# Kernel tuning notes

Measured on AMD Instinct MI355X. Metric: run time of the kernel, lower is better.

## Reference

```python
import jax, jax.numpy as jnp
import numpy as np

D_MODEL = 256
NHEAD = 8
HEAD_DIM = D_MODEL // NHEAD
EPS_ATTN = 1e-6
EPS_LN = 1e-5


def layer_norm(x, g, b):
    mu = jnp.mean(x, axis=-1, keepdims=True)
    var = jnp.mean(jnp.square(x - mu), axis=-1, keepdims=True)
    return (x - mu) * jax.lax.rsqrt(var + EPS_LN) * g + b


def setup_inputs() -> dict:
    key = jax.random.key(0)
    ks = jax.random.split(key, 9)
    N, L, S = 8, 8192, 8192
    d = D_MODEL
    sc = 1.0 / np.sqrt(d)
    return {
        "x": jax.random.normal(ks[0], (N, L, d), dtype=jnp.float32),
        "source": jax.random.normal(ks[1], (N, S, d), dtype=jnp.float32),
        "Wq": jax.random.normal(ks[2], (d, d), dtype=jnp.float32) * sc,
        "Wk": jax.random.normal(ks[3], (d, d), dtype=jnp.float32) * sc,
        "Wv": jax.random.normal(ks[4], (d, d), dtype=jnp.float32) * sc,
        "Wm": jax.random.normal(ks[5], (d, d), dtype=jnp.float32) * sc,
        "W1": jax.random.normal(ks[6], (2 * d, d), dtype=jnp.float32) * (1.0 / np.sqrt(2 * d)),
        "W2": jax.random.normal(ks[7], (d, d), dtype=jnp.float32) * sc,
        "g1": jnp.ones((d,), jnp.float32),
        "b1": jnp.zeros((d,), jnp.float32),
        "g2": jnp.ones((d,), jnp.float32),
        "b2": jnp.zeros((d,), jnp.float32),
    }


def linear_attention(q, k, v):
    # q: [N,L,H,D], k,v: [N,S,H,D]
    Q = jax.nn.elu(q) + 1.0
    K = jax.nn.elu(k) + 1.0
    S = v.shape[1]
    v = v / S
    KV = jnp.einsum('nshd,nshv->nhdv', K, v)          # [N,H,D,D]
    Z = 1.0 / (jnp.einsum('nlhd,nhd->nlh', Q, K.sum(axis=1)) + EPS_ATTN)
    out = jnp.einsum('nlhd,nhdv,nlh->nlhv', Q, KV, Z) * S
    return out


def reference(x, source, Wq, Wk, Wv, Wm, W1, W2, g1, b1, g2, b2):
    N, L, _ = x.shape
    q = (x @ Wq).reshape(N, L, NHEAD, HEAD_DIM)
    k = (source @ Wk).reshape(N, -1, NHEAD, HEAD_DIM)
    v = (source @ Wv).reshape(N, -1, NHEAD, HEAD_DIM)
    msg = linear_attention(q, k, v).reshape(N, L, D_MODEL)
    msg = layer_norm(msg @ Wm, g1, b1)
    msg = jnp.concatenate([x, msg], axis=2)
    msg = jax.nn.relu(msg @ W1) @ W2
    msg = layer_norm(msg, g2, b2)
    return x + msg
```

## Files before the change

kernel.cpp:

```cpp
#include <hip/hip_runtime.h>

typedef __attribute__((ext_vector_type(4))) float f32x4;
typedef __attribute__((ext_vector_type(8))) short short8;
typedef __attribute__((ext_vector_type(4))) unsigned short us4;
typedef __attribute__((ext_vector_type(8))) unsigned short us8;

#define D_MODEL 256
#define SEQ 8192L
#define NBATCH 8
#define TOTROWS 65536L

__device__ inline unsigned short f2bf(float f){
  unsigned int u = __float_as_uint(f);
  u += 0x7fffu + ((u >> 16) & 1u);
  return (unsigned short)(u >> 16);
}
__device__ inline float bf2f(unsigned short h){
  return __uint_as_float(((unsigned int)h) << 16);
}
__device__ inline f32x4 mfma16(short8 a, short8 b, f32x4 c){
  return __builtin_amdgcn_mfma_f32_16x16x32_bf16(a, b, c, 0, 0, 0);
}
__device__ inline us8 pack8(f32x4 a, f32x4 b){
  us8 o;
  o[0]=f2bf(a[0]); o[1]=f2bf(a[1]); o[2]=f2bf(a[2]); o[3]=f2bf(a[3]);
  o[4]=f2bf(b[0]); o[5]=f2bf(b[1]); o[6]=f2bf(b[2]); o[7]=f2bf(b[3]);
  return o;
}
__device__ inline void gl16(const unsigned short* g, unsigned short* lds){
  __builtin_amdgcn_global_load_lds(
      (const __attribute__((address_space(1))) unsigned int*)g,
      (__attribute__((address_space(3))) unsigned int*)lds, 16, 0, 0);
}

__global__ __launch_bounds__(256) void conv_f32_to_bf16(
    const float* __restrict__ s, unsigned short* __restrict__ d){
  const long N = TOTROWS * 256 / 8;
  for(long c = (long)blockIdx.x * 256 + threadIdx.x; c < N;
      c += (long)gridDim.x * 256){
    long off = c * 8;
    f32x4 v0 = *(const f32x4*)(s + off);
    f32x4 v1 = *(const f32x4*)(s + off + 4);
    *(us8*)(d + off) = pack8(v0, v1);
  }
}

__global__ void prep_weights(const float* __restrict__ Wq, const float* __restrict__ Wk,
                             const float* __restrict__ Wv, const float* __restrict__ Wm,
                             const float* __restrict__ W1, const float* __restrict__ W2,
                             unsigned short* __restrict__ WT){
  int o = blockIdx.x * 256 + threadIdx.x;
  int m = o >> 16, rem = o & 65535, n = rem >> 8, k = rem & 255;
  const float* s;
  switch(m){
    case 0: s = Wq; break;
    case 1: s = Wk; break;
    case 2: s = Wv; break;
    case 3: s = Wm; break;
    case 4: s = W1; break;
    case 5: s = W1 + 65536; break;
    default: s = W2; break;
  }
  WT[o] = f2bf(s[k * 256 + n]);
}

__global__ __launch_bounds__(256) void kv_proj(
    const unsigned short* __restrict__ srcb, const unsigned short* __restrict__ WT,
    unsigned short* __restrict__ Kw, unsigned short* __restrict__ Vw)
{
  __shared__ unsigned short As[128][32];
  __shared__ unsigned short Bs[128][32];
  const int t = threadIdx.x, lane = t & 63, wid = t >> 6;
  const int l16 = lane & 15, g4 = lane >> 4;
  const int wr = (wid >> 1) * 64, wc = (wid & 1) * 64;
  const int mb = blockIdx.x, nb = blockIdx.y;
  const long rowbase = (long)mb * 128;
  const unsigned short* Wsl = WT + (nb < 2 ? 1 : 2) * 65536 + (nb & 1) * 128 * 256;
  const int sr = lane >> 2, sc = (lane & 3) * 8;

  f32x4 acc[4][4] = {};
  for(int kb = 0; kb < 256; kb += 32){
    #pragma unroll
    for(int j = 0; j < 2; j++){
      int r0 = wid * 32 + j * 16;
      gl16(srcb + (rowbase + r0 + sr) * 256 + kb + sc, &As[r0][0]);
      gl16(Wsl  + (long)(r0 + sr) * 256 + kb + sc,     &Bs[r0][0]);
    }
    __syncthreads();
    short8 afr[4], bfr[4];
    #pragma unroll
    for(int mi = 0; mi < 4; mi++) afr[mi] = *(const short8*)&As[wr + mi*16 + l16][g4*8];
    #pragma unroll
    for(int ni = 0; ni < 4; ni++) bfr[ni] = *(const short8*)&Bs[wc + ni*16 + l16][g4*8];
    #pragma unroll
    for(int mi = 0; mi < 4; mi++)
      #pragma unroll
      for(int ni = 0; ni < 4; ni++)
        acc[mi][ni] = mfma16(afr[mi], bfr[ni], acc[mi][ni]);
    __syncthreads();
  }

  const bool isK = nb < 2;
  unsigned short* dst = isK ? Kw : Vw;
  const int colbase = (nb & 1) * 128 + wc;
  #pragma unroll
  for(int mi = 0; mi < 4; mi++)
    #pragma unroll
    for(int ni = 0; ni < 4; ni++)
      #pragma unroll
      for(int rr = 0; rr < 4; rr++){
        long row = rowbase + wr + mi*16 + g4*4 + rr;
        int col = colbase + ni*16 + l16;
        float v = acc[mi][ni][rr];
        v = isK ? (v > 0.f ? v + 1.f : __expf(v)) : v * (1.f / 8192.f);
        dst[row * 256 + col] = f2bf(v);
      }
}

__global__ __launch_bounds__(256) void kv_acc(const unsigned short* __restrict__ Kw,
                                              const unsigned short* __restrict__ Vw,
                                              float* __restrict__ part){
  const int c = blockIdx.x;
  const int n = blockIdx.y;
  const int t = threadIdx.x;
  const int h = t >> 5, d = t & 31;
  const long base = ((long)n * SEQ + (long)c * 128) * 256;
  float acc[32];
  #pragma unroll
  for(int j = 0; j < 32; j++) acc[j] = 0.f;
  float ks = 0.f;
  for(int rr = 0; rr < 128; rr++){
    const unsigned short* Kr = Kw + base + (long)rr * 256;
    const unsigned short* Vr = Vw + base + (long)rr * 256;
    float kv = bf2f(Kr[h * 32 + d]);
    ks += kv;
    #pragma unroll
    for(int q = 0; q < 4; q++){
      us8 vv = *(const us8*)(Vr + h * 32 + q * 8);
      #pragma unroll
      for(int j = 0; j < 8; j++) acc[q*8 + j] += kv * bf2f(vv[j]);
    }
  }
  float* p = part + ((long)(n * 64 + c) * 33) * 256;
  #pragma unroll
  for(int v = 0; v < 32; v++) p[v * 256 + t] = acc[v];
  p[32 * 256 + t] = ks;
}

__global__ void kv_red(const float* __restrict__ part, float* __restrict__ KVws){
  const int v = blockIdx.x;
  const int n = blockIdx.y;
  const int t = threadIdx.x;
  float s = 0.f;
  for(int c = 0; c < 64; c++) s += part[((long)(n * 64 + c) * 33 + v) * 256 + t];
  KVws[((long)n * 33 + v) * 256 + t] = s;
}

__global__ __launch_bounds__(256) void attn_kern(
    const unsigned short* __restrict__ xb, const unsigned short* __restrict__ WT,
    const float* __restrict__ KVws, const float* __restrict__ g1,
    const float* __restrict__ b1, unsigned short* __restrict__ msgln)
{
  __shared__ unsigned short As[64][32];
  __shared__ unsigned short Bu[256][32];
  __shared__ float zs[64][8];
  __shared__ float ksl[256];
  __shared__ unsigned short R[64][264];

  const int t = threadIdx.x, lane = t & 63, wid = t >> 6;
  const int l16 = lane & 15, g4 = lane >> 4;
  const int wc = wid * 64;
  const int mb = blockIdx.x;
  const long rowbase = (long)mb * 64;
  const int n = mb >> 7;
  const int sr = lane >> 2, sc = (lane & 3) * 8;

  f32x4 acc[4][4] = {};
  {
    const unsigned short* wq = WT;
    for(int kb = 0; kb < 256; kb += 32){
      gl16(xb + (rowbase + wid*16 + sr) * 256 + kb + sc, &As[wid*16][0]);
      #pragma unroll
      for(int j = 0; j < 4; j++){
        int r0 = wid * 64 + j * 16;
        gl16(wq + (long)(r0 + sr) * 256 + kb + sc, &Bu[r0][0]);
      }
      __syncthreads();
      short8 afr[4], bfr[4];
      #pragma unroll
      for(int mi = 0; mi < 4; mi++) afr[mi] = *(const short8*)&As[mi*16 + l16][g4*8];
      #pragma unroll
      for(int ni = 0; ni < 4; ni++) bfr[ni] = *(const short8*)&Bu[wc + ni*16 + l16][g4*8];
      #pragma unroll
      for(int mi = 0; mi < 4; mi++)
        #pragma unroll
        for(int ni = 0; ni < 4; ni++)
          acc[mi][ni] = mfma16(afr[mi], bfr[ni], acc[mi][ni]);
      __syncthreads();
    }
  }

  #pragma unroll
  for(int mi = 0; mi < 4; mi++)
    #pragma unroll
    for(int ni = 0; ni < 4; ni++)
      #pragma unroll
      for(int rr = 0; rr < 4; rr++){
        float v = acc[mi][ni][rr];
        v = v > 0.f ? v + 1.f : __expf(v);
        R[mi*16 + g4*4 + rr][wc + ni*16 + l16] = f2bf(v);
      }

  {
    const float* kvn = KVws + (long)n * 33 * 256;
    const int vv = t & 31, hh = t >> 5;
    #pragma unroll
    for(int d = 0; d < 32; d += 4){
      f32x4 w = *(const f32x4*)(kvn + vv * 256 + hh * 32 + d);
      us4 o; o[0]=f2bf(w[0]); o[1]=f2bf(w[1]); o[2]=f2bf(w[2]); o[3]=f2bf(w[3]);
      *(us4*)&Bu[t][d] = o;
    }
    ksl[t] = kvn[32 * 256 + t];
  }
  __syncthreads();

  #pragma unroll
  for(int pp = 0; pp < 2; pp++){
    int p = t + pp * 256;
    int row = p >> 3, h = p & 7;
    float s = 0.f;
    #pragma unroll
    for(int d = 0; d < 32; d++) s += bf2f(R[row][h*32 + d]) * ksl[h*32 + d];
    zs[row][h] = 1.f / (s + 1e-6f);
  }
  __syncthreads();

  f32x4 acc2[4][4];
  #pragma unroll
  for(int ni = 0; ni < 4; ni++){
    const int cb = wc + ni * 16;
    const int h = cb >> 5;
    short8 b = *(const short8*)&Bu[cb + l16][g4*8];
    #pragma unroll
    for(int mi = 0; mi < 4; mi++){
      short8 a = *(const short8*)&R[mi*16 + l16][h*32 + g4*8];
      f32x4 zz = {0.f, 0.f, 0.f, 0.f};
      acc2[mi][ni] = mfma16(a, b, zz);
    }
  }
  #pragma unroll
  for(int mi = 0; mi < 4; mi++)
    #pragma unroll
    for(int ni = 0; ni < 4; ni++){
      const int h = (wc + ni * 16) >> 5;
      #pragma unroll
      for(int rr = 0; rr < 4; rr++){
        int row = mi*16 + g4*4 + rr;
        acc2[mi][ni][rr] *= zs[row][h] * 8192.f;
      }
    }
  __syncthreads();
  #pragma unroll
  for(int mi = 0; mi < 4; mi++)
    #pragma unroll
    for(int ni = 0; ni < 4; ni++)
      #pragma unroll
      for(int rr = 0; rr < 4; rr++)
        R[mi*16 + g4*4 + rr][wc + ni*16 + l16] = f2bf(acc2[mi][ni][rr]);
  __syncthreads();

  f32x4 acc3[4][4] = {};
  {
    const unsigned short* wm = WT + 3 * 65536;
    for(int kb = 0; kb < 256; kb += 32){
      #pragma unroll
      for(int j = 0; j < 4; j++){
        int r0 = wid * 64 + j * 16;
        gl16(wm + (long)(r0 + sr) * 256 + kb + sc, &Bu[r0][0]);
      }
      __syncthreads();
      short8 afr[4], bfr[4];
      #pragma unroll
      for(int mi = 0; mi < 4; mi++) afr[mi] = *(const short8*)&R[mi*16 + l16][kb + g4*8];
      #pragma unroll
      for(int ni = 0; ni < 4; ni++) bfr[ni] = *(const short8*)&Bu[wc + ni*16 + l16][g4*8];
      #pragma unroll
      for(int mi = 0; mi < 4; mi++)
        #pragma unroll
        for(int ni = 0; ni < 4; ni++)
          acc3[mi][ni] = mfma16(afr[mi], bfr[ni], acc3[mi][ni]);
      __syncthreads();
    }
  }

  #pragma unroll
  for(int mi = 0; mi < 4; mi++)
    #pragma unroll
    for(int ni = 0; ni < 4; ni++)
      #pragma unroll
      for(int rr = 0; rr < 4; rr++)
        R[mi*16 + g4*4 + rr][wc + ni*16 + l16] = f2bf(acc3[mi][ni][rr]);
  __syncthreads();

  {
    int row = t >> 2, q = t & 3;
    float s = 0.f, ss = 0.f;
    #pragma unroll
    for(int j8 = 0; j8 < 8; j8++){
      us8 vv = *(const us8*)&R[row][q*64 + j8*8];
      #pragma unroll
      for(int e = 0; e < 8; e++){ float v = bf2f(vv[e]); s += v; ss += v * v; }
    }
    s  += __shfl_xor(s, 1);  ss += __shfl_xor(ss, 1);
    s  += __shfl_xor(s, 2);  ss += __shfl_xor(ss, 2);
    float mu  = s * (1.f / 256.f);
    float var = ss * (1.f / 256.f) - mu * mu;
    float rs  = rsqrtf(var + 1e-5f);
    unsigned short* orow = msgln + (rowbase + row) * 256 + q * 64;
    const float* g1p = g1 + q * 64;
    const float* b1p = b1 + q * 64;
    #pragma unroll
    for(int j8 = 0; j8 < 8; j8++){
      us8 vv = *(const us8*)&R[row][q*64 + j8*8];
      us8 o;
      #pragma unroll
      for(int e = 0; e < 8; e++){
        float v = (bf2f(vv[e]) - mu) * rs * g1p[j8*8 + e] + b1p[j8*8 + e];
        o[e] = f2bf(v);
      }
      *(us8*)(orow + j8*8) = o;
    }
  }
}

__global__ __launch_bounds__(256) void ffn_kern(
    const float* __restrict__ x, const unsigned short* __restrict__ xb,
    const unsigned short* __restrict__ WT,
    const unsigned short* __restrict__ msgln, const float* __restrict__ g2,
    const float* __restrict__ b2, float* __restrict__ out)
{
  __shared__ unsigned short As[64][32];
  __shared__ unsigned short Bs[256][32];
  __shared__ unsigned short R[64][264];
  const int t = threadIdx.x, lane = t & 63, wid = t >> 6;
  const int l16 = lane & 15, g4 = lane >> 4;
  const int wc = wid * 64;
  const long rowbase = (long)blockIdx.x * 64;
  const int sr = lane >> 2, sc = (lane & 3) * 8;

  f32x4 acc[4][4] = {};
  for(int it = 0; it < 16; it++){
    int kb = (it & 7) * 32;
    const unsigned short* asrc = (it < 8) ? xb : msgln;
    gl16(asrc + (rowbase + wid*16 + sr) * 256 + kb + sc, &As[wid*16][0]);
    const unsigned short* wsl = WT + (it < 8 ? 4 : 5) * 65536;
    #pragma unroll
    for(int j = 0; j < 4; j++){
      int r0 = wid * 64 + j * 16;
      gl16(wsl + (long)(r0 + sr) * 256 + kb + sc, &Bs[r0][0]);
    }
    __syncthreads();
    short8 afr[4], bfr[4];
    #pragma unroll
    for(int mi = 0; mi < 4; mi++) afr[mi] = *(const short8*)&As[mi*16 + l16][g4*8];
    #pragma unroll
    for(int ni = 0; ni < 4; ni++) bfr[ni] = *(const short8*)&Bs[wc + ni*16 + l16][g4*8];
    #pragma unroll
    for(int mi = 0; mi < 4; mi++)
      #pragma unroll
      for(int ni = 0; ni < 4; ni++)
        acc[mi][ni] = mfma16(afr[mi], bfr[ni], acc[mi][ni]);
    __syncthreads();
  }

  #pragma unroll
  for(int mi = 0; mi < 4; mi++)
    #pragma unroll
    for(int ni = 0; ni < 4; ni++)
      #pragma unroll
      for(int rr = 0; rr < 4; rr++){
        float v = acc[mi][ni][rr];
        R[mi*16 + g4*4 + rr][wc + ni*16 + l16] = f2bf(v > 0.f ? v : 0.f);
      }
  __syncthreads();

  f32x4 acc2[4][4] = {};
  {
    const unsigned short* w2 = WT + 6 * 65536;
    for(int kb = 0; kb < 256; kb += 32){
      #pragma unroll
      for(int j = 0; j < 4; j++){
        int r0 = wid * 64 + j * 16;
        gl16(w2 + (long)(r0 + sr) * 256 + kb + sc, &Bs[r0][0]);
      }
      __syncthreads();
      short8 afr[4], bfr[4];
      #pragma unroll
      for(int mi = 0; mi < 4; mi++) afr[mi] = *(const short8*)&R[mi*16 + l16][kb + g4*8];
      #pragma unroll
      for(int ni = 0; ni < 4; ni++) bfr[ni] = *(const short8*)&Bs[wc + ni*16 + l16][g4*8];
      #pragma unroll
      for(int mi = 0; mi < 4; mi++)
        #pragma unroll
        for(int ni = 0; ni < 4; ni++)
          acc2[mi][ni] = mfma16(afr[mi], bfr[ni], acc2[mi][ni]);
      __syncthreads();
    }
  }

  #pragma unroll
  for(int mi = 0; mi < 4; mi++)
    #pragma unroll
    for(int ni = 0; ni < 4; ni++)
      #pragma unroll
      for(int rr = 0; rr < 4; rr++)
        R[mi*16 + g4*4 + rr][wc + ni*16 + l16] = f2bf(acc2[mi][ni][rr]);
  __syncthreads();

  {
    int row = t >> 2, q = t & 3;
    float s = 0.f, ss = 0.f;
    #pragma unroll
    for(int j8 = 0; j8 < 8; j8++){
      us8 vv = *(const us8*)&R[row][q*64 + j8*8];
      #pragma unroll
      for(int e = 0; e < 8; e++){ float v = bf2f(vv[e]); s += v; ss += v * v; }
    }
    s  += __shfl_xor(s, 1);  ss += __shfl_xor(ss, 1);
    s  += __shfl_xor(s, 2);  ss += __shfl_xor(ss, 2);
    float mu  = s * (1.f / 256.f);
    float var = ss * (1.f / 256.f) - mu * mu;
    float rs  = rsqrtf(var + 1e-5f);
    const float* xr = x + (rowbase + row) * 256 + q * 64;
    float* orow = out + (rowbase + row) * 256 + q * 64;
    const float* g2p = g2 + q * 64;
    const float* b2p = b2 + q * 64;
    #pragma unroll
    for(int j4 = 0; j4 < 16; j4++){
      f32x4 xv = *(const f32x4*)(xr + j4 * 4);
      f32x4 o;
      #pragma unroll
      for(int e = 0; e < 4; e++){
        int idx = j4 * 4 + e;
        float v = (bf2f(R[row][q*64 + idx]) - mu) * rs * g2p[idx] + b2p[idx];
        o[e] = xv[e] + v;
      }
      *(f32x4*)(orow + j4 * 4) = o;
    }
  }
}

extern "C" void kernel_launch(void* const* d_in, const int* in_sizes, int n_in,
                              void* d_out, int out_size, void* d_ws, size_t ws_size,
                              hipStream_t stream)
{
  const float* x   = (const float*)d_in[0];
  const float* src = (const float*)d_in[1];
  const float* Wq  = (const float*)d_in[2];
  const float* Wk  = (const float*)d_in[3];
  const float* Wv  = (const float*)d_in[4];
  const float* Wm  = (const float*)d_in[5];
  const float* W1  = (const float*)d_in[6];
  const float* W2  = (const float*)d_in[7];
  const float* g1  = (const float*)d_in[8];
  const float* b1  = (const float*)d_in[9];
  const float* g2  = (const float*)d_in[10];
  const float* b2  = (const float*)d_in[11];

  char* ws = (char*)d_ws;
  unsigned short* WT   = (unsigned short*)(ws);
  unsigned short* srcb = (unsigned short*)(ws + (1ul  << 20));
  float*          part = (float*)         (ws + (1ul  << 20));
  unsigned short* xb   = (unsigned short*)(ws + (1ul  << 20));
  unsigned short* Kw   = (unsigned short*)(ws + (33ul << 20));
  unsigned short* msgl = Kw;
  unsigned short* Vw   = (unsigned short*)(ws + (65ul << 20));
  float*          KVws = (float*)         (ws + (97ul << 20));

  prep_weights<<<1792, 256, 0, stream>>>(Wq, Wk, Wv, Wm, W1, W2, WT);
  conv_f32_to_bf16<<<2048, 256, 0, stream>>>(src, srcb);
  kv_proj<<<dim3(512, 4), 256, 0, stream>>>(srcb, WT, Kw, Vw);
  kv_acc<<<dim3(64, 8), 256, 0, stream>>>(Kw, Vw, part);
  kv_red<<<dim3(33, 8), 256, 0, stream>>>(part, KVws);
  conv_f32_to_bf16<<<2048, 256, 0, stream>>>(x, xb);
  attn_kern<<<1024, 256, 0, stream>>>(xb, WT, KVws, g1, b1, msgl);
  ffn_kern<<<1024, 256, 0, stream>>>(x, xb, WT, msgl, g2, b2, (float*)d_out);
}
```

Baseline: 415.8 us.

## Double-buffer LDS tiles in projection, attention and FFN GEMM loops

Converts the k-loops of kv_proj, attn_kern and ffn_kern to a two-buffer shared-memory pipeline. Each iteration issues the next tile's global-to-LDS loads into the other buffer before doing the MFMAs on the current one, which removes one barrier per iteration. The Wm and W2 tiles for the second GEMM are prefetched during the preceding epilogue. This roughly doubles the staging LDS per block, which may lower occupancy, especially in attn_kern.

```diff
diff --git a/kernel.cpp b/kernel.cpp
--- a/kernel.cpp
+++ b/kernel.cpp
@@ -68,8 +68,8 @@
     const unsigned short* __restrict__ srcb, const unsigned short* __restrict__ WT,
     unsigned short* __restrict__ Kw, unsigned short* __restrict__ Vw)
 {
-  __shared__ unsigned short As[128][32];
-  __shared__ unsigned short Bs[128][32];
+  __shared__ unsigned short As[2][128][32];
+  __shared__ unsigned short Bs[2][128][32];
   const int t = threadIdx.x, lane = t & 63, wid = t >> 6;
   const int l16 = lane & 15, g4 = lane >> 4;
   const int wr = (wid >> 1) * 64, wc = (wid & 1) * 64;
@@ -78,26 +78,33 @@
   const unsigned short* Wsl = WT + (nb < 2 ? 1 : 2) * 65536 + (nb & 1) * 128 * 256;
   const int sr = lane >> 2, sc = (lane & 3) * 8;
 
-  f32x4 acc[4][4] = {};
-  for(int kb = 0; kb < 256; kb += 32){
+  auto STAGE = [&](int buf, int kb){
     #pragma unroll
     for(int j = 0; j < 2; j++){
       int r0 = wid * 32 + j * 16;
-      gl16(srcb + (rowbase + r0 + sr) * 256 + kb + sc, &As[r0][0]);
-      gl16(Wsl  + (long)(r0 + sr) * 256 + kb + sc,     &Bs[r0][0]);
-    }
-    __syncthreads();
+      gl16(srcb + (rowbase + r0 + sr) * 256 + kb + sc, &As[buf][r0][0]);
+      gl16(Wsl  + (long)(r0 + sr) * 256 + kb + sc,     &Bs[buf][r0][0]);
+    }
+  };
+
+  f32x4 acc[4][4] = {};
+  STAGE(0, 0);
+  __syncthreads();
+  int cur = 0;
+  for(int it = 0; it < 8; it++){
+    if(it < 7) STAGE(cur ^ 1, (it + 1) * 32);
     short8 afr[4], bfr[4];
     #pragma unroll
-    for(int mi = 0; mi < 4; mi++) afr[mi] = *(const short8*)&As[wr + mi*16 + l16][g4*8];
-    #pragma unroll
-    for(int ni = 0; ni < 4; ni++) bfr[ni] = *(const short8*)&Bs[wc + ni*16 + l16][g4*8];
+    for(int mi = 0; mi < 4; mi++) afr[mi] = *(const short8*)&As[cur][wr + mi*16 + l16][g4*8];
+    #pragma unroll
+    for(int ni = 0; ni < 4; ni++) bfr[ni] = *(const short8*)&Bs[cur][wc + ni*16 + l16][g4*8];
     #pragma unroll
     for(int mi = 0; mi < 4; mi++)
       #pragma unroll
       for(int ni = 0; ni < 4; ni++)
         acc[mi][ni] = mfma16(afr[mi], bfr[ni], acc[mi][ni]);
     __syncthreads();
+    cur ^= 1;
   }
 
   const bool isK = nb < 2;
@@ -161,8 +168,8 @@
     const float* __restrict__ KVws, const float* __restrict__ g1,
     const float* __restrict__ b1, unsigned short* __restrict__ msgln)
 {
-  __shared__ unsigned short As[64][32];
-  __shared__ unsigned short Bu[256][32];
+  __shared__ unsigned short As[2][64][32];
+  __shared__ unsigned short Bu[2][256][32];
   __shared__ float zs[64][8];
   __shared__ float ksl[256];
   __shared__ unsigned short R[64][264];
@@ -175,29 +182,43 @@
   const int n = mb >> 7;
   const int sr = lane >> 2, sc = (lane & 3) * 8;
 
+  const unsigned short* wq = WT;
+  const unsigned short* wm = WT + 3 * 65536;
+
+  auto STAGE1 = [&](int buf, int kb){
+    gl16(xb + (rowbase + wid*16 + sr) * 256 + kb + sc, &As[buf][wid*16][0]);
+    #pragma unroll
+    for(int j = 0; j < 4; j++){
+      int r0 = wid * 64 + j * 16;
+      gl16(wq + (long)(r0 + sr) * 256 + kb + sc, &Bu[buf][r0][0]);
+    }
+  };
+  auto STAGE6 = [&](int buf, int kb){
+    #pragma unroll
+    for(int j = 0; j < 4; j++){
+      int r0 = wid * 64 + j * 16;
+      gl16(wm + (long)(r0 + sr) * 256 + kb + sc, &Bu[buf][r0][0]);
+    }
+  };
+
   f32x4 acc[4][4] = {};
-  {
-    const unsigned short* wq = WT;
-    for(int kb = 0; kb < 256; kb += 32){
-      gl16(xb + (rowbase + wid*16 + sr) * 256 + kb + sc, &As[wid*16][0]);
-      #pragma unroll
-      for(int j = 0; j < 4; j++){
-        int r0 = wid * 64 + j * 16;
-        gl16(wq + (long)(r0 + sr) * 256 + kb + sc, &Bu[r0][0]);
-      }
-      __syncthreads();
-      short8 afr[4], bfr[4];
-      #pragma unroll
-      for(int mi = 0; mi < 4; mi++) afr[mi] = *(const short8*)&As[mi*16 + l16][g4*8];
-      #pragma unroll
-      for(int ni = 0; ni < 4; ni++) bfr[ni] = *(const short8*)&Bu[wc + ni*16 + l16][g4*8];
-      #pragma unroll
-      for(int mi = 0; mi < 4; mi++)
-        #pragma unroll
-        for(int ni = 0; ni < 4; ni++)
-          acc[mi][ni] = mfma16(afr[mi], bfr[ni], acc[mi][ni]);
-      __syncthreads();
-    }
+  STAGE1(0, 0);
+  __syncthreads();
+  int cur = 0;
+  for(int it = 0; it < 8; it++){
+    if(it < 7) STAGE1(cur ^ 1, (it + 1) * 32);
+    short8 afr[4], bfr[4];
+    #pragma unroll
+    for(int mi = 0; mi < 4; mi++) afr[mi] = *(const short8*)&As[cur][mi*16 + l16][g4*8];
+    #pragma unroll
+    for(int ni = 0; ni < 4; ni++) bfr[ni] = *(const short8*)&Bu[cur][wc + ni*16 + l16][g4*8];
+    #pragma unroll
+    for(int mi = 0; mi < 4; mi++)
+      #pragma unroll
+      for(int ni = 0; ni < 4; ni++)
+        acc[mi][ni] = mfma16(afr[mi], bfr[ni], acc[mi][ni]);
+    __syncthreads();
+    cur ^= 1;
   }
 
   #pragma unroll
@@ -218,7 +239,7 @@
     for(int d = 0; d < 32; d += 4){
       f32x4 w = *(const f32x4*)(kvn + vv * 256 + hh * 32 + d);
       us4 o; o[0]=f2bf(w[0]); o[1]=f2bf(w[1]); o[2]=f2bf(w[2]); o[3]=f2bf(w[3]);
-      *(us4*)&Bu[t][d] = o;
+      *(us4*)&Bu[0][t][d] = o;
     }
     ksl[t] = kvn[32 * 256 + t];
   }
@@ -240,7 +261,7 @@
   for(int ni = 0; ni < 4; ni++){
     const int cb = wc + ni * 16;
     const int h = cb >> 5;
-    short8 b = *(const short8*)&Bu[cb + l16][g4*8];
+    short8 b = *(const short8*)&Bu[0][cb + l16][g4*8];
     #pragma unroll
     for(int mi = 0; mi < 4; mi++){
       short8 a = *(const short8*)&R[mi*16 + l16][h*32 + g4*8];
@@ -248,6 +269,7 @@
       acc2[mi][ni] = mfma16(a, b, zz);
     }
   }
+  STAGE6(1, 0);
   #pragma unroll
   for(int mi = 0; mi < 4; mi++)
     #pragma unroll
@@ -270,27 +292,22 @@
   __syncthreads();
 
   f32x4 acc3[4][4] = {};
-  {
-    const unsigned short* wm = WT + 3 * 65536;
-    for(int kb = 0; kb < 256; kb += 32){
-      #pragma unroll
-      for(int j = 0; j < 4; j++){
-        int r0 = wid * 64 + j * 16;
-        gl16(wm + (long)(r0 + sr) * 256 + kb + sc, &Bu[r0][0]);
-      }
-      __syncthreads();
-      short8 afr[4], bfr[4];
-      #pragma unroll
-      for(int mi = 0; mi < 4; mi++) afr[mi] = *(const short8*)&R[mi*16 + l16][kb + g4*8];
-      #pragma unroll
-      for(int ni = 0; ni < 4; ni++) bfr[ni] = *(const short8*)&Bu[wc + ni*16 + l16][g4*8];
-      #pragma unroll
-      for(int mi = 0; mi < 4; mi++)
-        #pragma unroll
-        for(int ni = 0; ni < 4; ni++)
-          acc3[mi][ni] = mfma16(afr[mi], bfr[ni], acc3[mi][ni]);
-      __syncthreads();
-    }
+  cur = 1;
+  for(int it = 0; it < 8; it++){
+    if(it < 7) STAGE6(cur ^ 1, (it + 1) * 32);
+    int kb = it * 32;
+    short8 afr[4], bfr[4];
+    #pragma unroll
+    for(int mi = 0; mi < 4; mi++) afr[mi] = *(const short8*)&R[mi*16 + l16][kb + g4*8];
+    #pragma unroll
+    for(int ni = 0; ni < 4; ni++) bfr[ni] = *(const short8*)&Bu[cur][wc + ni*16 + l16][g4*8];
+    #pragma unroll
+    for(int mi = 0; mi < 4; mi++)
+      #pragma unroll
+      for(int ni = 0; ni < 4; ni++)
+        acc3[mi][ni] = mfma16(afr[mi], bfr[ni], acc3[mi][ni]);
+    __syncthreads();
+    cur ^= 1;
   }
 
   #pragma unroll
@@ -339,8 +356,8 @@
     const unsigned short* __restrict__ msgln, const float* __restrict__ g2,
     const float* __restrict__ b2, float* __restrict__ out)
 {
-  __shared__ unsigned short As[64][32];
-  __shared__ unsigned short Bs[256][32];
+  __shared__ unsigned short As[2][64][32];
+  __shared__ unsigned short Bs[2][256][32];
   __shared__ unsigned short R[64][264];
   const int t = threadIdx.x, lane = t & 63, wid = t >> 6;
   const int l16 = lane & 15, g4 = lane >> 4;
@@ -348,30 +365,46 @@
   const long rowbase = (long)blockIdx.x * 64;
   const int sr = lane >> 2, sc = (lane & 3) * 8;
 
-  f32x4 acc[4][4] = {};
-  for(int it = 0; it < 16; it++){
+  auto STAGE1 = [&](int buf, int it){
     int kb = (it & 7) * 32;
     const unsigned short* asrc = (it < 8) ? xb : msgln;
-    gl16(asrc + (rowbase + wid*16 + sr) * 256 + kb + sc, &As[wid*16][0]);
+    gl16(asrc + (rowbase + wid*16 + sr) * 256 + kb + sc, &As[buf][wid*16][0]);
     const unsigned short* wsl = WT + (it < 8 ? 4 : 5) * 65536;
     #pragma unroll
     for(int j = 0; j < 4; j++){
       int r0 = wid * 64 + j * 16;
-      gl16(wsl + (long)(r0 + sr) * 256 + kb + sc, &Bs[r0][0]);
-    }
-    __syncthreads();
+      gl16(wsl + (long)(r0 + sr) * 256 + kb + sc, &Bs[buf][r0][0]);
+    }
+  };
+  const unsigned short* w2 = WT + 6 * 65536;
+  auto STAGE2 = [&](int buf, int kb){
+    #pragma unroll
+    for(int j = 0; j < 4; j++){
+      int r0 = wid * 64 + j * 16;
+      gl16(w2 + (long)(r0 + sr) * 256 + kb + sc, &Bs[buf][r0][0]);
+    }
+  };
+
+  f32x4 acc[4][4] = {};
+  STAGE1(0, 0);
+  __syncthreads();
+  int cur = 0;
+  for(int it = 0; it < 16; it++){
+    if(it < 15) STAGE1(cur ^ 1, it + 1);
     short8 afr[4], bfr[4];
     #pragma unroll
-    for(int mi = 0; mi < 4; mi++) afr[mi] = *(const short8*)&As[mi*16 + l16][g4*8];
-    #pragma unroll
-    for(int ni = 0; ni < 4; ni++) bfr[ni] = *(const short8*)&Bs[wc + ni*16 + l16][g4*8];
+    for(int mi = 0; mi < 4; mi++) afr[mi] = *(const short8*)&As[cur][mi*16 + l16][g4*8];
+    #pragma unroll
+    for(int ni = 0; ni < 4; ni++) bfr[ni] = *(const short8*)&Bs[cur][wc + ni*16 + l16][g4*8];
     #pragma unroll
     for(int mi = 0; mi < 4; mi++)
       #pragma unroll
       for(int ni = 0; ni < 4; ni++)
         acc[mi][ni] = mfma16(afr[mi], bfr[ni], acc[mi][ni]);
     __syncthreads();
-  }
+    cur ^= 1;
+  }
+  STAGE2(0, 0);
 
   #pragma unroll
   for(int mi = 0; mi < 4; mi++)
@@ -385,27 +418,22 @@
   __syncthreads();
 
   f32x4 acc2[4][4] = {};
-  {
-    const unsigned short* w2 = WT + 6 * 65536;
-    for(int kb = 0; kb < 256; kb += 32){
-      #pragma unroll
-      for(int j = 0; j < 4; j++){
-        int r0 = wid * 64 + j * 16;
-        gl16(w2 + (long)(r0 + sr) * 256 + kb + sc, &Bs[r0][0]);
-      }
-      __syncthreads();
-      short8 afr[4], bfr[4];
-      #pragma unroll
-      for(int mi = 0; mi < 4; mi++) afr[mi] = *(const short8*)&R[mi*16 + l16][kb + g4*8];
-      #pragma unroll
-      for(int ni = 0; ni < 4; ni++) bfr[ni] = *(const short8*)&Bs[wc + ni*16 + l16][g4*8];
-      #pragma unroll
-      for(int mi = 0; mi < 4; mi++)
-        #pragma unroll
-        for(int ni = 0; ni < 4; ni++)
-          acc2[mi][ni] = mfma16(afr[mi], bfr[ni], acc2[mi][ni]);
-      __syncthreads();
-    }
+  cur = 0;
+  for(int it = 0; it < 8; it++){
+    if(it < 7) STAGE2(cur ^ 1, (it + 1) * 32);
+    int kb = it * 32;
+    short8 afr[4], bfr[4];
+    #pragma unroll
+    for(int mi = 0; mi < 4; mi++) afr[mi] = *(const short8*)&R[mi*16 + l16][kb + g4*8];
+    #pragma unroll
+    for(int ni = 0; ni < 4; ni++) bfr[ni] = *(const short8*)&Bs[cur][wc + ni*16 + l16][g4*8];
+    #pragma unroll
+    for(int mi = 0; mi < 4; mi++)
+      #pragma unroll
+      for(int ni = 0; ni < 4; ni++)
+        acc2[mi][ni] = mfma16(afr[mi], bfr[ni], acc2[mi][ni]);
+    __syncthreads();
+    cur ^= 1;
   }
 
   #pragma unroll
```

Result: no change. 419.9 us (+1.0%).

## Load GEMM operand fragments directly from global memory instead of LDS staging

Applied to the files above, without the earlier changes.

Replaces the global_load_lds staging of A and B tiles into shared memory in kv_proj, attn_kern and ffn_kern. Each wave now loads its MFMA fragments straight from global memory into registers inside fully unrolled K loops, with no per-iteration barriers. This drops LDS traffic and synchronisation and lets the compiler schedule loads across iterations. In exchange, each wave re-reads the weight and activation data it used to share through LDS (more cache and global traffic), makes strided 16-byte row accesses, and raises register pressure from the unrolling.

```diff
diff --git a/kernel.cpp b/kernel.cpp
--- a/kernel.cpp
+++ b/kernel.cpp
@@ -27,10 +27,8 @@
   o[4]=f2bf(b[0]); o[5]=f2bf(b[1]); o[6]=f2bf(b[2]); o[7]=f2bf(b[3]);
   return o;
 }
-__device__ inline void gl16(const unsigned short* g, unsigned short* lds){
-  __builtin_amdgcn_global_load_lds(
-      (const __attribute__((address_space(1))) unsigned int*)g,
-      (__attribute__((address_space(3))) unsigned int*)lds, 16, 0, 0);
+__device__ inline short8 g16(const unsigned short* p){
+  return *(const short8*)p;
 }
 
 __global__ __launch_bounds__(256) void conv_f32_to_bf16(
@@ -68,36 +66,29 @@
     const unsigned short* __restrict__ srcb, const unsigned short* __restrict__ WT,
     unsigned short* __restrict__ Kw, unsigned short* __restrict__ Vw)
 {
-  __shared__ unsigned short As[128][32];
-  __shared__ unsigned short Bs[128][32];
   const int t = threadIdx.x, lane = t & 63, wid = t >> 6;
   const int l16 = lane & 15, g4 = lane >> 4;
   const int wr = (wid >> 1) * 64, wc = (wid & 1) * 64;
   const int mb = blockIdx.x, nb = blockIdx.y;
   const long rowbase = (long)mb * 128;
   const unsigned short* Wsl = WT + (nb < 2 ? 1 : 2) * 65536 + (nb & 1) * 128 * 256;
-  const int sr = lane >> 2, sc = (lane & 3) * 8;
 
   f32x4 acc[4][4] = {};
-  for(int kb = 0; kb < 256; kb += 32){
-    #pragma unroll
-    for(int j = 0; j < 2; j++){
-      int r0 = wid * 32 + j * 16;
-      gl16(srcb + (rowbase + r0 + sr) * 256 + kb + sc, &As[r0][0]);
-      gl16(Wsl  + (long)(r0 + sr) * 256 + kb + sc,     &Bs[r0][0]);
-    }
-    __syncthreads();
-    short8 afr[4], bfr[4];
-    #pragma unroll
-    for(int mi = 0; mi < 4; mi++) afr[mi] = *(const short8*)&As[wr + mi*16 + l16][g4*8];
-    #pragma unroll
-    for(int ni = 0; ni < 4; ni++) bfr[ni] = *(const short8*)&Bs[wc + ni*16 + l16][g4*8];
+  #pragma unroll
+  for(int it = 0; it < 8; it++){
+    int kb = it * 32;
+    short8 a[4], b[4];
+    #pragma unroll
+    for(int mi = 0; mi < 4; mi++)
+      a[mi] = g16(srcb + (rowbase + wr + mi*16 + l16) * 256 + kb + g4*8);
+    #pragma unroll
+    for(int ni = 0; ni < 4; ni++)
+      b[ni] = g16(Wsl + (long)(wc + ni*16 + l16) * 256 + kb + g4*8);
     #pragma unroll
     for(int mi = 0; mi < 4; mi++)
       #pragma unroll
       for(int ni = 0; ni < 4; ni++)
-        acc[mi][ni] = mfma16(afr[mi], bfr[ni], acc[mi][ni]);
-    __syncthreads();
+        acc[mi][ni] = mfma16(a[mi], b[ni], acc[mi][ni]);
   }
 
   const bool isK = nb < 2;
@@ -161,8 +152,7 @@
     const float* __restrict__ KVws, const float* __restrict__ g1,
     const float* __restrict__ b1, unsigned short* __restrict__ msgln)
 {
-  __shared__ unsigned short As[64][32];
-  __shared__ unsigned short Bu[256][32];
+  __shared__ unsigned short kvB[256][32];
   __shared__ float zs[64][8];
   __shared__ float ksl[256];
   __shared__ unsigned short R[64][264];
@@ -173,31 +163,38 @@
   const int mb = blockIdx.x;
   const long rowbase = (long)mb * 64;
   const int n = mb >> 7;
-  const int sr = lane >> 2, sc = (lane & 3) * 8;
+
+  const unsigned short* wq = WT;
+  const unsigned short* wm = WT + 3 * 65536;
+
+  {
+    const float* kvn = KVws + (long)n * 33 * 256;
+    const int vv = t & 31, hh = t >> 5;
+    #pragma unroll
+    for(int d = 0; d < 32; d += 4){
+      f32x4 w = *(const f32x4*)(kvn + vv * 256 + hh * 32 + d);
+      us4 o; o[0]=f2bf(w[0]); o[1]=f2bf(w[1]); o[2]=f2bf(w[2]); o[3]=f2bf(w[3]);
+      *(us4*)&kvB[t][d] = o;
+    }
+    ksl[t] = kvn[32 * 256 + t];
+  }
 
   f32x4 acc[4][4] = {};
-  {
-    const unsigned short* wq = WT;
-    for(int kb = 0; kb < 256; kb += 32){
-      gl16(xb + (rowbase + wid*16 + sr) * 256 + kb + sc, &As[wid*16][0]);
-      #pragma unroll
-      for(int j = 0; j < 4; j++){
-        int r0 = wid * 64 + j * 16;
-        gl16(wq + (long)(r0 + sr) * 256 + kb + sc, &Bu[r0][0]);
-      }
-      __syncthreads();
-      short8 afr[4], bfr[4];
-      #pragma unroll
-      for(int mi = 0; mi < 4; mi++) afr[mi] = *(const short8*)&As[mi*16 + l16][g4*8];
-      #pragma unroll
-      for(int ni = 0; ni < 4; ni++) bfr[ni] = *(const short8*)&Bu[wc + ni*16 + l16][g4*8];
-      #pragma unroll
-      for(int mi = 0; mi < 4; mi++)
-        #pragma unroll
-        for(int ni = 0; ni < 4; ni++)
-          acc[mi][ni] = mfma16(afr[mi], bfr[ni], acc[mi][ni]);
-      __syncthreads();
-    }
+  #pragma unroll
+  for(int it = 0; it < 8; it++){
+    int kb = it * 32;
+    short8 a[4], b[4];
+    #pragma unroll
+    for(int mi = 0; mi < 4; mi++)
+      a[mi] = g16(xb + (rowbase + mi*16 + l16) * 256 + kb + g4*8);
+    #pragma unroll
+    for(int ni = 0; ni < 4; ni++)
+      b[ni] = g16(wq + (long)(wc + ni*16 + l16) * 256 + kb + g4*8);
+    #pragma unroll
+    for(int mi = 0; mi < 4; mi++)
+      #pragma unroll
+      for(int ni = 0; ni < 4; ni++)
+        acc[mi][ni] = mfma16(a[mi], b[ni], acc[mi][ni]);
   }
 
   #pragma unroll
@@ -210,18 +207,6 @@
         v = v > 0.f ? v + 1.f : __expf(v);
         R[mi*16 + g4*4 + rr][wc + ni*16 + l16] = f2bf(v);
       }
-
-  {
-    const float* kvn = KVws + (long)n * 33 * 256;
-    const int vv = t & 31, hh = t >> 5;
-    #pragma unroll
-    for(int d = 0; d < 32; d += 4){
-      f32x4 w = *(const f32x4*)(kvn + vv * 256 + hh * 32 + d);
-      us4 o; o[0]=f2bf(w[0]); o[1]=f2bf(w[1]); o[2]=f2bf(w[2]); o[3]=f2bf(w[3]);
-      *(us4*)&Bu[t][d] = o;
-    }
-    ksl[t] = kvn[32 * 256 + t];
-  }
   __syncthreads();
 
   #pragma unroll
@@ -240,7 +225,7 @@
   for(int ni = 0; ni < 4; ni++){
     const int cb = wc + ni * 16;
     const int h = cb >> 5;
-    short8 b = *(const short8*)&Bu[cb + l16][g4*8];
+    short8 b = *(const short8*)&kvB[cb + l16][g4*8];
     #pragma unroll
     for(int mi = 0; mi < 4; mi++){
       short8 a = *(const short8*)&R[mi*16 + l16][h*32 + g4*8];
@@ -270,28 +255,23 @@
   __syncthreads();
 
   f32x4 acc3[4][4] = {};
-  {
-    const unsigned short* wm = WT + 3 * 65536;
-    for(int kb = 0; kb < 256; kb += 32){
-      #pragma unroll
-      for(int j = 0; j < 4; j++){
-        int r0 = wid * 64 + j * 16;
-        gl16(wm + (long)(r0 + sr) * 256 + kb + sc, &Bu[r0][0]);
-      }
-      __syncthreads();
-      short8 afr[4], bfr[4];
-      #pragma unroll
-      for(int mi = 0; mi < 4; mi++) afr[mi] = *(const short8*)&R[mi*16 + l16][kb + g4*8];
-      #pragma unroll
-      for(int ni = 0; ni < 4; ni++) bfr[ni] = *(const short8*)&Bu[wc + ni*16 + l16][g4*8];
-      #pragma unroll
-      for(int mi = 0; mi < 4; mi++)
-        #pragma unroll
-        for(int ni = 0; ni < 4; ni++)
-          acc3[mi][ni] = mfma16(afr[mi], bfr[ni], acc3[mi][ni]);
-      __syncthreads();
-    }
-  }
+  #pragma unroll
+  for(int it = 0; it < 8; it++){
+    int kb = it * 32;
+    short8 afr[4], b[4];
+    #pragma unroll
+    for(int mi = 0; mi < 4; mi++)
+      afr[mi] = *(const short8*)&R[mi*16 + l16][kb + g4*8];
+    #pragma unroll
+    for(int ni = 0; ni < 4; ni++)
+      b[ni] = g16(wm + (long)(wc + ni*16 + l16) * 256 + kb + g4*8);
+    #pragma unroll
+    for(int mi = 0; mi < 4; mi++)
+      #pragma unroll
+      for(int ni = 0; ni < 4; ni++)
+        acc3[mi][ni] = mfma16(afr[mi], b[ni], acc3[mi][ni]);
+  }
+  __syncthreads();
 
   #pragma unroll
   for(int mi = 0; mi < 4; mi++)
@@ -339,38 +319,32 @@
     const unsigned short* __restrict__ msgln, const float* __restrict__ g2,
     const float* __restrict__ b2, float* __restrict__ out)
 {
-  __shared__ unsigned short As[64][32];
-  __shared__ unsigned short Bs[256][32];
   __shared__ unsigned short R[64][264];
   const int t = threadIdx.x, lane = t & 63, wid = t >> 6;
   const int l16 = lane & 15, g4 = lane >> 4;
   const int wc = wid * 64;
   const long rowbase = (long)blockIdx.x * 64;
-  const int sr = lane >> 2, sc = (lane & 3) * 8;
+
+  const unsigned short* w2 = WT + 6 * 65536;
 
   f32x4 acc[4][4] = {};
+  #pragma unroll
   for(int it = 0; it < 16; it++){
     int kb = (it & 7) * 32;
     const unsigned short* asrc = (it < 8) ? xb : msgln;
-    gl16(asrc + (rowbase + wid*16 + sr) * 256 + kb + sc, &As[wid*16][0]);
     const unsigned short* wsl = WT + (it < 8 ? 4 : 5) * 65536;
-    #pragma unroll
-    for(int j = 0; j < 4; j++){
-      int r0 = wid * 64 + j * 16;
-      gl16(wsl + (long)(r0 + sr) * 256 + kb + sc, &Bs[r0][0]);
-    }
-    __syncthreads();
-    short8 afr[4], bfr[4];
-    #pragma unroll
-    for(int mi = 0; mi < 4; mi++) afr[mi] = *(const short8*)&As[mi*16 + l16][g4*8];
-    #pragma unroll
-    for(int ni = 0; ni < 4; ni++) bfr[ni] = *(const short8*)&Bs[wc + ni*16 + l16][g4*8];
+    short8 a[4], b[4];
+    #pragma unroll
+    for(int mi = 0; mi < 4; mi++)
+      a[mi] = g16(asrc + (rowbase + mi*16 + l16) * 256 + kb + g4*8);
+    #pragma unroll
+    for(int ni = 0; ni < 4; ni++)
+      b[ni] = g16(wsl + (long)(wc + ni*16 + l16) * 256 + kb + g4*8);
     #pragma unroll
     for(int mi = 0; mi < 4; mi++)
       #pragma unroll
       for(int ni = 0; ni < 4; ni++)
-        acc[mi][ni] = mfma16(afr[mi], bfr[ni], acc[mi][ni]);
-    __syncthreads();
+        acc[mi][ni] = mfma16(a[mi], b[ni], acc[mi][ni]);
   }
 
   #pragma unroll
@@ -385,28 +359,23 @@
   __syncthreads();
 
   f32x4 acc2[4][4] = {};
-  {
-    const unsigned short* w2 = WT + 6 * 65536;
-    for(int kb = 0; kb < 256; kb += 32){
-      #pragma unroll
-      for(int j = 0; j < 4; j++){
-        int r0 = wid * 64 + j * 16;
-        gl16(w2 + (long)(r0 + sr) * 256 + kb + sc, &Bs[r0][0]);
-      }
-      __syncthreads();
-      short8 afr[4], bfr[4];
-      #pragma unroll
-      for(int mi = 0; mi < 4; mi++) afr[mi] = *(const short8*)&R[mi*16 + l16][kb + g4*8];
-      #pragma unroll
-      for(int ni = 0; ni < 4; ni++) bfr[ni] = *(const short8*)&Bs[wc + ni*16 + l16][g4*8];
-      #pragma unroll
-      for(int mi = 0; mi < 4; mi++)
-        #pragma unroll
-        for(int ni = 0; ni < 4; ni++)
-          acc2[mi][ni] = mfma16(afr[mi], bfr[ni], acc2[mi][ni]);
-      __syncthreads();
-    }
-  }
+  #pragma unroll
+  for(int it = 0; it < 8; it++){
+    int kb = it * 32;
+    short8 afr[4], b[4];
+    #pragma unroll
+    for(int mi = 0; mi < 4; mi++)
+      afr[mi] = *(const short8*)&R[mi*16 + l16][kb + g4*8];
+    #pragma unroll
+    for(int ni = 0; ni < 4; ni++)
+      b[ni] = g16(w2 + (long)(wc + ni*16 + l16) * 256 + kb + g4*8);
+    #pragma unroll
+    for(int mi = 0; mi < 4; mi++)
+      #pragma unroll
+      for(int ni = 0; ni < 4; ni++)
+        acc2[mi][ni] = mfma16(afr[mi], b[ni], acc2[mi][ni]);
+  }
+  __syncthreads();
 
   #pragma unroll
   for(int mi = 0; mi < 4; mi++)
```

After: 499.5 us. 20.1% more time.
